# Optimization experiments

Hardware: AMD Instinct MI355X
Metric: run time of the kernel (lower is better)

The kernel has to match this reference:

```python
import jax, jax.numpy as jnp
import numpy as np

B, N, DIM = 16, 3136, 512
HEADS, AGENT, WINDOW = 8, 49, 14


def setup_inputs() -> dict:
    key = jax.random.key(0)
    ks = jax.random.split(key, 14)
    s = 0.02
    return {
        "x": jax.random.normal(ks[0], (B, N, DIM), jnp.float32),
        "w_qkv": jax.random.normal(ks[1], (3 * DIM, DIM), jnp.float32) * 0.02,
        "w_proj": jax.random.normal(ks[2], (DIM, DIM), jnp.float32) * 0.02,
        "b_proj": jnp.zeros((DIM,), jnp.float32),
        "w_dwc": jax.random.normal(ks[3], (DIM, 1, 3, 3), jnp.float32) * 0.1,
        "b_dwc": jnp.zeros((DIM,), jnp.float32),
        "an_bias": jax.random.normal(ks[4], (HEADS, AGENT, 7, 7), jnp.float32) * s,
        "na_bias": jax.random.normal(ks[5], (HEADS, AGENT, 7, 7), jnp.float32) * s,
        "ah_bias": jax.random.normal(ks[6], (1, HEADS, AGENT, WINDOW, 1), jnp.float32) * s,
        "aw_bias": jax.random.normal(ks[7], (1, HEADS, AGENT, 1, WINDOW), jnp.float32) * s,
        "ha_bias": jax.random.normal(ks[8], (1, HEADS, WINDOW, 1, AGENT), jnp.float32) * s,
        "wa_bias": jax.random.normal(ks[9], (1, HEADS, 1, WINDOW, AGENT), jnp.float32) * s,
        "ca_bias": jax.random.normal(ks[10], (1, HEADS, 1, AGENT), jnp.float32) * s,
    }


def reference(x, w_qkv, w_proj, b_proj, w_dwc, b_dwc, an_bias, na_bias,
              ah_bias, aw_bias, ha_bias, wa_bias, ca_bias):
    b, n, c = x.shape
    h = w = int(np.sqrt(n))            # 56x56, static
    nh, hd = HEADS, c // HEADS
    scale = hd ** -0.5
    ww = WINDOW * WINDOW               # 196

    qkv = x @ w_qkv.T                  # (b, n, 3c)
    q, k, v = jnp.split(qkv, 3, axis=-1)

    # agent tokens: adaptive avg-pool q to (7, 7)  (exact block mean, 56/7=8)
    pool = int(AGENT ** 0.5)
    q_img = q.reshape(b, h, w, c).transpose(0, 3, 1, 2)  # (b, c, h, w)
    pooled = q_img.reshape(b, c, pool, h // pool, pool, w // pool).mean(axis=(3, 5))
    agent = pooled.reshape(b, c, AGENT).transpose(0, 2, 1)  # (b, 49, c)

    qh = q.reshape(b, n, nh, hd).transpose(0, 2, 1, 3)      # (b, H, n, d)
    kh = k.reshape(b, n, nh, hd).transpose(0, 2, 1, 3)
    vh = v.reshape(b, n, nh, hd).transpose(0, 2, 1, 3)
    ah = agent.reshape(b, AGENT, nh, hd).transpose(0, 2, 1, 3)  # (b, H, 49, d)

    # ---- stage 1: agent -> kv attention ----
    pb1 = jax.image.resize(an_bias, (nh, AGENT, WINDOW, WINDOW), 'bilinear')
    pb1 = pb1.reshape(1, nh, AGENT, ww)
    pb2 = (ah_bias + aw_bias).reshape(1, nh, AGENT, ww)
    pb = jnp.broadcast_to(pb1 + pb2, (b, nh, AGENT, ww))
    scores1 = jnp.einsum('bhad,bhnd->bhan', ah * scale, kh)     # (b, H, 49, n)
    pb_up = jax.image.resize(pb, scores1.shape, 'bilinear')     # 196 -> n along last dim
    attn1 = jax.nn.softmax(scores1 + pb_up, axis=-1)
    agent_v = jnp.einsum('bhan,bhnd->bhad', attn1, vh)          # (b, H, 49, d)

    # ---- stage 2: query -> agent attention ----
    ab1 = jax.image.resize(na_bias, (nh, AGENT, WINDOW, WINDOW), 'bilinear')
    ab1 = ab1.reshape(1, nh, AGENT, ww).transpose(0, 1, 3, 2)   # (1, H, 196, 49)
    ab2 = (ha_bias + wa_bias).reshape(1, nh, ww, AGENT)
    ab = jnp.broadcast_to(ab1 + ab2, (b, nh, ww, AGENT))
    ab = jnp.concatenate([jnp.broadcast_to(ca_bias, (b, nh, 1, AGENT)), ab], axis=-2)
    scores2 = jnp.einsum('bhnd,bhad->bhna', qh * scale, ah)     # (b, H, n, 49)
    ab_up = jax.image.resize(ab, scores2.shape, 'bilinear')     # 197 -> n along dim -2
    attn2 = jax.nn.softmax(scores2 + ab_up, axis=-1)
    out = jnp.einsum('bhna,bhad->bhnd', attn2, agent_v)
    out = out.transpose(0, 2, 1, 3).reshape(b, n, c)

    # ---- depthwise-conv residual on v ----
    v_img = vh.transpose(0, 2, 1, 3).reshape(b, h, w, c).transpose(0, 3, 1, 2)
    dwc = jax.lax.conv_general_dilated(
        v_img, w_dwc, (1, 1), 'SAME',
        dimension_numbers=('NCHW', 'OIHW', 'NCHW'), feature_group_count=c)
    dwc = dwc + b_dwc[None, :, None, None]
    out = out + dwc.transpose(0, 2, 3, 1).reshape(b, n, c)

    return out @ w_proj.T + b_proj
```

## Files before the change

### kernel.cpp

```cpp
#include <hip/hip_runtime.h>

typedef unsigned short u16;
typedef unsigned int   u32;
typedef unsigned long long u64;
typedef float  f32x4  __attribute__((ext_vector_type(4)));
typedef __bf16 bf16x8 __attribute__((ext_vector_type(8)));

#define DEV static __device__ __forceinline__

DEV float bf2f(u16 u){ union{float f;u32 i;}v; v.i=((u32)u)<<16; return v.f; }
DEV float bflo(u32 u){ union{float f;u32 i;}v; v.i=u<<16; return v.f; }
DEV float bfhi(u32 u){ union{float f;u32 i;}v; v.i=u&0xffff0000u; return v.f; }
DEV u16   f2bf(float f){ union{float f;u32 i;}v; v.f=f; return (u16)((v.i + 0x7fffu + ((v.i>>16)&1u))>>16); }

DEV void async16(const void* g, void* l){
  __builtin_amdgcn_global_load_lds((const __attribute__((address_space(1))) void*)g,
                                   (__attribute__((address_space(3))) void*)l, 16, 0, 0);
}

__global__ __launch_bounds__(256) void cast_bf16(const float* __restrict__ in,
                                                 u16* __restrict__ out, int n4)
{
  int i = blockIdx.x*256 + threadIdx.x;
  if (i >= n4) return;
  float4 v = ((const float4*)in)[i];
  ushort4 o;
  o.x = f2bf(v.x); o.y = f2bf(v.y); o.z = f2bf(v.z); o.w = f2bf(v.w);
  ((ushort4*)out)[i] = o;
}

__global__ __launch_bounds__(256) void gemm_bt(
    const u16* __restrict__ A, const u16* __restrict__ W, int K, int mode,
    u16* __restrict__ oq, u16* __restrict__ okk, u16* __restrict__ ov,
    float* __restrict__ of, const float* __restrict__ bias)
{
  __shared__ __align__(16) u16 As[4096];
  __shared__ __align__(16) u16 Bs[4096];
  const int tid  = threadIdx.x;
  const int wave = tid >> 6, lane = tid & 63;
  const int wm = wave >> 1, wn = wave & 1;
  const int r16 = lane & 15, q4 = lane >> 4;
  const size_t Abase = (size_t)blockIdx.x * 128 * K;
  const size_t Bbase = (size_t)blockIdx.y * 128 * K;

  f32x4 acc[4][4];
  #pragma unroll
  for (int i=0;i<4;i++)
    #pragma unroll
    for (int j=0;j<4;j++) acc[i][j] = (f32x4){0.f,0.f,0.f,0.f};

  for (int k0 = 0; k0 < K; k0 += 32) {
    #pragma unroll
    for (int i=0;i<2;i++){
      int c   = wave*128 + i*64 + lane;
      int row = c >> 2, kc = (c & 3) * 8;
      async16(A + Abase + (size_t)row*K + k0 + kc, (char*)As + (wave*128 + i*64)*16);
      async16(W + Bbase + (size_t)row*K + k0 + kc, (char*)Bs + (wave*128 + i*64)*16);
    }
    __syncthreads();
    bf16x8 af[4], bfr[4];
    #pragma unroll
    for (int i=0;i<4;i++) af[i]  = *(const bf16x8*)&As[(wm*64 + i*16 + r16)*32 + q4*8];
    #pragma unroll
    for (int j=0;j<4;j++) bfr[j] = *(const bf16x8*)&Bs[(wn*64 + j*16 + r16)*32 + q4*8];
    #pragma unroll
    for (int i=0;i<4;i++)
      #pragma unroll
      for (int j=0;j<4;j++)
        acc[i][j] = __builtin_amdgcn_mfma_f32_16x16x32_bf16(af[i], bfr[j], acc[i][j], 0,0,0);
    __syncthreads();
  }

  const int m0 = blockIdx.x*128 + wm*64;
  const int n0 = blockIdx.y*128 + wn*64;
  #pragma unroll
  for (int i=0;i<4;i++)
    #pragma unroll
    for (int j=0;j<4;j++)
      #pragma unroll
      for (int r=0;r<4;r++){
        int m = m0 + i*16 + q4*4 + r;
        int n = n0 + j*16 + r16;
        float val = acc[i][j][r];
        if (mode == 0){
          int sel = n >> 9, col = n & 511;
          u16* dst = sel==0 ? oq : (sel==1 ? okk : ov);
          dst[(size_t)m*512 + col] = f2bf(val);
        } else {
          of[(size_t)m*512 + n] = val + bias[n];
        }
      }
}

__global__ __launch_bounds__(256) void pool_q(const u16* __restrict__ qb, u16* __restrict__ agentb)
{
  int idx = blockIdx.x*256 + threadIdx.x;
  int c = idx & 511;
  int ba = idx >> 9;
  int a = ba & 63, b = ba >> 6;
  if (a >= 49) { agentb[idx] = 0; return; }
  int ay = a / 7, ax = a % 7;
  const u16* base = qb + (size_t)b*3136*512 + c;
  float acc = 0.f;
  #pragma unroll
  for (int iy=0; iy<8; iy++){
    int rowoff = ((ay*8 + iy)*56 + ax*8) * 512;
    #pragma unroll
    for (int ix=0; ix<8; ix++) acc += bf2f(base[(size_t)rowoff + ix*512]);
  }
  agentb[idx] = f2bf(acc * 0.015625f);
}

DEV void lin1(float c, int S, int& i0, int& i1, float& w){
  if (c <= 0.f){ i0=0; i1=0; w=0.f; }
  else if (c >= (float)(S-1)){ i0=S-1; i1=S-1; w=0.f; }
  else { i0=(int)c; i1=i0+1; w=c-(float)i0; }
}
DEV float bilin7(const float* s, int Y, int X){
  int y0,y1,x0,x1; float wy,wx;
  lin1(0.5f*Y - 0.25f, 7, y0,y1,wy);
  lin1(0.5f*X - 0.25f, 7, x0,x1,wx);
  float v0 = s[y0*7+x0] + wx*(s[y0*7+x1]-s[y0*7+x0]);
  float v1 = s[y1*7+x0] + wx*(s[y1*7+x1]-s[y1*7+x0]);
  return v0 + wy*(v1 - v0);
}
__global__ __launch_bounds__(256) void bias_pre(
    const float* __restrict__ an_bias, const float* __restrict__ na_bias,
    const float* __restrict__ ah_bias, const float* __restrict__ aw_bias,
    const float* __restrict__ ha_bias, const float* __restrict__ wa_bias,
    const float* __restrict__ ca_bias, float* __restrict__ PB, float* __restrict__ AB)
{
  int idx = blockIdx.x*256 + threadIdx.x;
  if (idx < 8*49*196){
    int j = idx % 196; int ha = idx / 196; int a = ha % 49, h = ha / 49;
    int wy = j / 14, wx = j % 14;
    PB[idx] = bilin7(an_bias + (h*49+a)*49, wy, wx)
            + ah_bias[(h*49+a)*14 + wy] + aw_bias[(h*49+a)*14 + wx];
  }
  int idx2 = idx - 8*49*196;
  if (idx2 >= 0 && idx2 < 8*197*49){
    int a = idx2 % 49; int hr = idx2 / 49; int r = hr % 197, h = hr / 197;
    float v;
    if (r == 0) v = ca_bias[h*49 + a];
    else {
      int j = r - 1; int wy = j / 14, wx = j % 14;
      v = bilin7(na_bias + (h*49+a)*49, wy, wx)
        + ha_bias[(h*14+wy)*49 + a] + wa_bias[(h*14+wx)*49 + a];
    }
    AB[idx2] = v;
  }
}

__global__ __launch_bounds__(256) void pbit_expand(const float* __restrict__ PB, float* __restrict__ PBIT)
{
  int idx = blockIdx.x*256 + threadIdx.x;
  if (idx >= 1605632) return;
  int a = idx & 63; int t = idx >> 6; int n = t % 3136; int h = t / 3136;
  float val = -1e30f;
  if (a < 49) {
    const float* row = PB + (h*49 + a)*196;
    float c1 = (n + 0.5f)*0.0625f - 0.5f;
    if (c1 <= 0.f) val = row[0];
    else if (c1 >= 195.f) val = row[195];
    else { int j0 = (int)c1; float w = c1 - (float)j0; val = row[j0] + w*(row[j0+1]-row[j0]); }
  }
  PBIT[idx] = val;
}

__global__ __launch_bounds__(256) void abi_expand(const float* __restrict__ AB, float* __restrict__ ABI)
{
  int idx = blockIdx.x*256 + threadIdx.x;
  if (idx >= 1605632) return;
  int a = idx & 63; int t = idx >> 6; int n = t % 3136; int h = t / 3136;
  float val = -1e30f;
  if (a < 49) {
    float c2 = (n + 0.5f)*(197.0f/3136.0f) - 0.5f;
    int r0; float w;
    if (c2 <= 0.f) { r0 = 0; w = 0.f; }
    else if (c2 >= 196.f) { r0 = 196; w = 0.f; }
    else { r0 = (int)c2; w = c2 - (float)r0; }
    int r1 = (r0 < 196) ? r0 + 1 : 196;
    float v0 = AB[(h*197 + r0)*49 + a];
    float v1 = AB[(h*197 + r1)*49 + a];
    val = v0 + w*(v1 - v0);
  }
  ABI[idx] = val;
}

__global__ __launch_bounds__(256) void stage1_mfma(
    const u16* __restrict__ kb, const u16* __restrict__ vb,
    const u16* __restrict__ agentb, const float* __restrict__ PBIT,
    float* __restrict__ pav, float* __restrict__ psum)
{
  int bh = blockIdx.x, chunk = blockIdx.y;
  int b = bh >> 3, h = bh & 7;
  int tid = threadIdx.x, lane = tid & 63, w = tid >> 6;
  int r16 = lane & 15, q4 = lane >> 4;
  __shared__ __align__(16) u16 kld[64*64];
  __shared__ __align__(16) u16 vt[64*68];
  __shared__ __align__(16) u16 scb[64*72];

  int agent = w*16 + r16;
  bf16x8 bah[2];
  {
    const u16* ap = agentb + ((size_t)(b*64 + agent))*512 + h*64 + q4*8;
    bah[0] = *(const bf16x8*)ap;
    bah[1] = *(const bf16x8*)(ap + 32);
  }
  f32x4 Oacc[4];
  #pragma unroll
  for (int nt = 0; nt < 4; nt++) Oacc[nt] = (f32x4){0.f,0.f,0.f,0.f};
  float ssum = 0.f;
  int n0 = chunk * 448;
  const u16* kbase = kb + ((size_t)b*3136)*512 + h*64;
  const u16* vbase = vb + ((size_t)b*3136)*512 + h*64;

  for (int it = 0; it < 7; it++) {
    int nt0 = n0 + it*64;
    __syncthreads();
    #pragma unroll
    for (int i = 0; i < 2; i++) {
      int L = w*128 + i*64 + lane;
      int row = L >> 3, colc = (L & 7) ^ (row & 7);
      async16(kbase + (size_t)(nt0 + row)*512 + colc*8, (char*)kld + (w*128 + i*64)*16);
    }
    uint4 va[2]; int vtok[2], vdc[2];
    #pragma unroll
    for (int i = 0; i < 2; i++) {
      int c = tid + i*256;
      vtok[i] = c >> 3; vdc[i] = (c & 7)*8;
      va[i] = *(const uint4*)(vbase + (size_t)(nt0 + vtok[i])*512 + vdc[i]);
    }
    #pragma unroll
    for (int i = 0; i < 2; i++) {
      u32 uu[4] = {va[i].x, va[i].y, va[i].z, va[i].w};
      #pragma unroll
      for (int e = 0; e < 4; e++) {
        vt[(vdc[i] + 2*e + 0)*68 + vtok[i]] = (u16)(uu[e] & 0xffffu);
        vt[(vdc[i] + 2*e + 1)*68 + vtok[i]] = (u16)(uu[e] >> 16);
      }
    }
    __syncthreads();
    f32x4 S[4];
    #pragma unroll
    for (int mt = 0; mt < 4; mt++) S[mt] = (f32x4){0.f,0.f,0.f,0.f};
    #pragma unroll
    for (int ks = 0; ks < 2; ks++)
      #pragma unroll
      for (int mt = 0; mt < 4; mt++) {
        int row = mt*16 + r16;
        int colc = (ks*4 + q4) ^ (row & 7);
        bf16x8 afr = *(const bf16x8*)&kld[row*64 + colc*8];
        S[mt] = __builtin_amdgcn_mfma_f32_16x16x32_bf16(afr, bah[ks], S[mt], 0,0,0);
      }
    #pragma unroll
    for (int mt = 0; mt < 4; mt++) {
      u64 pk = 0;
      #pragma unroll
      for (int r = 0; r < 4; r++) {
        int tokl = mt*16 + q4*4 + r;
        float bias = PBIT[((size_t)h*3136 + nt0 + tokl)*64 + agent];
        float e = __expf(0.125f*S[mt][r] + bias);
        ssum += e;
        pk |= ((u64)f2bf(e)) << (16*r);
      }
      *(u64*)&scb[agent*72 + mt*16 + q4*4] = pk;
    }
    #pragma unroll
    for (int ks = 0; ks < 2; ks++) {
      bf16x8 ap = *(const bf16x8*)&scb[agent*72 + ks*32 + q4*8];
      #pragma unroll
      for (int nt = 0; nt < 4; nt++) {
        union { bf16x8 v; uint2 u[2]; } bb;
        int dim = nt*16 + r16;
        bb.u[0] = *(const uint2*)&vt[dim*68 + ks*32 + q4*8];
        bb.u[1] = *(const uint2*)&vt[dim*68 + ks*32 + q4*8 + 4];
        Oacc[nt] = __builtin_amdgcn_mfma_f32_16x16x32_bf16(ap, bb.v, Oacc[nt], 0,0,0);
      }
    }
  }
  ssum += __shfl_xor(ssum, 16);
  ssum += __shfl_xor(ssum, 32);
  size_t pb = (size_t)chunk*128 + bh;
  #pragma unroll
  for (int nt = 0; nt < 4; nt++)
    #pragma unroll
    for (int r = 0; r < 4; r++)
      pav[(pb*64 + (w*16 + q4*4 + r))*64 + nt*16 + r16] = Oacc[nt][r];
  if (lane < 16) psum[pb*64 + w*16 + lane] = ssum;
}

__global__ __launch_bounds__(256) void reduce_agv(
    const float* __restrict__ pav, const float* __restrict__ psum, u16* __restrict__ avTg)
{
  int idx = blockIdx.x*256 + threadIdx.x;
  int d = idx & 63, a = (idx >> 6) & 63, bh = idx >> 12;
  float val = 0.f;
  if (a < 49) {
    float acc = 0.f, s = 0.f;
    #pragma unroll
    for (int c = 0; c < 7; c++) {
      acc += pav[(((size_t)c*128 + bh)*64 + a)*64 + d];
      s   += psum[((size_t)c*128 + bh)*64 + a];
    }
    val = acc / s;
  }
  avTg[((size_t)bh*64 + d)*72 + a] = f2bf(val);
}

__global__ __launch_bounds__(256) void stage2_mfma(
    const u16* __restrict__ qb, const u16* __restrict__ agentb,
    const u16* __restrict__ avTg, const float* __restrict__ ABI,
    u16* __restrict__ aout)
{
  int bh = blockIdx.x, chunk = blockIdx.y;
  int b = bh >> 3, h = bh & 7;
  int tid = threadIdx.x, lane = tid & 63, w = tid >> 6;
  int r16 = lane & 15, q4 = lane >> 4;
  __shared__ __align__(16) u16 avs[64*72];
  __shared__ __align__(16) u16 scb2[4*16*72];

  const u16* avsrc = avTg + (size_t)bh*4608;
  #pragma unroll
  for (int rr = 0; rr < 3; rr++) {
    int c = rr*256 + w*64 + lane;
    if (c < 576) async16(avsrc + c*8, (char*)avs + ((size_t)rr*256 + w*64)*16);
  }
  bf16x8 bah[4][2];
  #pragma unroll
  for (int nt = 0; nt < 4; nt++) {
    const u16* ap = agentb + ((size_t)(b*64 + nt*16 + r16))*512 + h*64 + q4*8;
    bah[nt][0] = *(const bf16x8*)ap;
    bah[nt][1] = *(const bf16x8*)(ap + 32);
  }
  __syncthreads();

  u16* scw = scb2 + w*16*72;
  for (int t = 0; t < 7; t++) {
    int tok0 = (chunk*28 + w*7 + t)*16;
    bf16x8 aq[2];
    {
      const u16* qp = qb + ((size_t)b*3136 + tok0 + r16)*512 + h*64 + q4*8;
      aq[0] = *(const bf16x8*)qp;
      aq[1] = *(const bf16x8*)(qp + 32);
    }
    f32x4 S[4];
    #pragma unroll
    for (int nt = 0; nt < 4; nt++) S[nt] = (f32x4){0.f,0.f,0.f,0.f};
    #pragma unroll
    for (int ks = 0; ks < 2; ks++)
      #pragma unroll
      for (int nt = 0; nt < 4; nt++)
        S[nt] = __builtin_amdgcn_mfma_f32_16x16x32_bf16(aq[ks], bah[nt][ks], S[nt], 0,0,0);
    float rs[4] = {0.f,0.f,0.f,0.f};
    #pragma unroll
    for (int nt = 0; nt < 4; nt++)
      #pragma unroll
      for (int r = 0; r < 4; r++) {
        int tokl = q4*4 + r;
        float bias = ABI[((size_t)h*3136 + tok0 + tokl)*64 + nt*16 + r16];
        float e = __expf(0.125f*S[nt][r] + bias);
        rs[r] += e;
        scw[tokl*72 + nt*16 + r16] = f2bf(e);
      }
    #pragma unroll
    for (int m = 1; m <= 8; m <<= 1)
      #pragma unroll
      for (int r = 0; r < 4; r++) rs[r] += __shfl_xor(rs[r], m);
    f32x4 O[4];
    #pragma unroll
    for (int nt = 0; nt < 4; nt++) O[nt] = (f32x4){0.f,0.f,0.f,0.f};
    #pragma unroll
    for (int ks = 0; ks < 2; ks++) {
      bf16x8 ap2 = *(const bf16x8*)&scw[r16*72 + ks*32 + q4*8];
      #pragma unroll
      for (int nt = 0; nt < 4; nt++) {
        bf16x8 bv = *(const bf16x8*)&avs[(nt*16 + r16)*72 + ks*32 + q4*8];
        O[nt] = __builtin_amdgcn_mfma_f32_16x16x32_bf16(ap2, bv, O[nt], 0,0,0);
      }
    }
    float inv[4];
    #pragma unroll
    for (int r = 0; r < 4; r++) inv[r] = 1.0f / rs[r];
    #pragma unroll
    for (int nt = 0; nt < 4; nt++)
      #pragma unroll
      for (int r = 0; r < 4; r++)
        aout[((size_t)b*3136 + tok0 + q4*4 + r)*512 + h*64 + nt*16 + r16] = f2bf(O[nt][r]*inv[r]);
  }
}

__global__ __launch_bounds__(256) void dwc_add2(
    const u16* __restrict__ vb, const float* __restrict__ w_dwc,
    const float* __restrict__ b_dwc, u16* __restrict__ io)
{
  int wave = (blockIdx.x << 2) + (threadIdx.x >> 6);
  int lane = threadIdx.x & 63;
  int c0 = lane * 8;

  float wt[9][8];
  {
    float tmp[72];
    const float4* wp = (const float4*)(w_dwc + c0*9);
    #pragma unroll
    for (int i = 0; i < 18; i++) {
      float4 v4 = wp[i];
      tmp[4*i] = v4.x; tmp[4*i+1] = v4.y; tmp[4*i+2] = v4.z; tmp[4*i+3] = v4.w;
    }
    #pragma unroll
    for (int j = 0; j < 8; j++)
      #pragma unroll
      for (int tp = 0; tp < 9; tp++) wt[tp][j] = tmp[j*9 + tp];
  }
  float bias[8];
  {
    const float4* bp = (const float4*)(b_dwc + c0);
    float4 a4 = bp[0], b4 = bp[1];
    bias[0]=a4.x; bias[1]=a4.y; bias[2]=a4.z; bias[3]=a4.w;
    bias[4]=b4.x; bias[5]=b4.y; bias[6]=b4.z; bias[7]=b4.w;
  }

  int t0 = wave * 16;
  int b = t0 / 3136;
  int n0 = t0 - b*3136;
  const u16* vbase = vb + ((size_t)b*3136)*512 + c0;

  for (int ti = 0; ti < 16; ti++) {
    int n = n0 + ti;
    int y = n / 56, x = n - y*56;
    size_t toff = ((size_t)b*3136 + n)*512 + c0;
    float acc[8];
    {
      uint4 uo = *(const uint4*)(io + toff);
      u32 uu[4] = {uo.x, uo.y, uo.z, uo.w};
      #pragma unroll
      for (int e = 0; e < 4; e++) {
        acc[2*e+0] = bflo(uu[e]) + bias[2*e+0];
        acc[2*e+1] = bfhi(uu[e]) + bias[2*e+1];
      }
    }
    #pragma unroll
    for (int dy = 0; dy < 3; dy++) {
      int yy = y + dy - 1;
      if (yy < 0 || yy > 55) continue;
      #pragma unroll
      for (int dx = 0; dx < 3; dx++) {
        int xx = x + dx - 1;
        if (xx < 0 || xx > 55) continue;
        uint4 uv = *(const uint4*)(vbase + ((size_t)(yy*56 + xx) << 9));
        u32 uu[4] = {uv.x, uv.y, uv.z, uv.w};
        const float* wr = wt[dy*3 + dx];
        #pragma unroll
        for (int e = 0; e < 4; e++) {
          acc[2*e+0] += bflo(uu[e]) * wr[2*e+0];
          acc[2*e+1] += bfhi(uu[e]) * wr[2*e+1];
        }
      }
    }
    uint4 pk;
    pk.x = (u32)f2bf(acc[0]) | ((u32)f2bf(acc[1]) << 16);
    pk.y = (u32)f2bf(acc[2]) | ((u32)f2bf(acc[3]) << 16);
    pk.z = (u32)f2bf(acc[4]) | ((u32)f2bf(acc[5]) << 16);
    pk.w = (u32)f2bf(acc[6]) | ((u32)f2bf(acc[7]) << 16);
    *(uint4*)(io + toff) = pk;
  }
}

extern "C" void kernel_launch(void* const* d_in, const int* in_sizes, int n_in,
                              void* d_out, int out_size, void* d_ws, size_t ws_size,
                              hipStream_t stream)
{
  const float* x       = (const float*)d_in[0];
  const float* w_qkv   = (const float*)d_in[1];
  const float* w_proj  = (const float*)d_in[2];
  const float* b_proj  = (const float*)d_in[3];
  const float* w_dwc   = (const float*)d_in[4];
  const float* b_dwc   = (const float*)d_in[5];
  const float* an_bias = (const float*)d_in[6];
  const float* na_bias = (const float*)d_in[7];
  const float* ah_bias = (const float*)d_in[8];
  const float* aw_bias = (const float*)d_in[9];
  const float* ha_bias = (const float*)d_in[10];
  const float* wa_bias = (const float*)d_in[11];
  const float* ca_bias = (const float*)d_in[12];

  if (ws_size < 210000000u) return;

  char* p = (char*)d_ws;
  u16* regA   = (u16*)p;  p += 51380224;
  u16* qb     = (u16*)p;  p += 51380224;
  u16* kb     = (u16*)p;  p += 51380224;
  u16* vb     = (u16*)p;  p += 51380224;
  u16* wqkvb  = (u16*)p;  p += 1572864;
  u16* wprojb = (u16*)p;  p += 524288;
  u16* agentb = (u16*)p;  p += 1048576;
  float* PB   = (float*)p; p += 307456;
  float* AB   = (float*)p; p += 309248;

  float* PBIT = (float*)((char*)regA);
  float* ABI  = (float*)((char*)regA + 6422528);
  float* pav  = (float*)((char*)regA + 12845056);
  float* psum = (float*)((char*)regA + 27525120);
  u16*   avTg = (u16*)  ((char*)regA + 27754496);
  u16*   aout = kb;

  cast_bf16<<<25088, 256, 0, stream>>>(x, regA, 6422528);
  cast_bf16<<<768,   256, 0, stream>>>(w_qkv, wqkvb, 196608);
  cast_bf16<<<256,   256, 0, stream>>>(w_proj, wprojb, 65536);

  gemm_bt<<<dim3(392,12), 256, 0, stream>>>(regA, wqkvb, 512, 0, qb, kb, vb, nullptr, nullptr);
  pool_q<<<2048, 256, 0, stream>>>(qb, agentb);
  bias_pre<<<602, 256, 0, stream>>>(an_bias, na_bias, ah_bias, aw_bias, ha_bias, wa_bias, ca_bias, PB, AB);
  pbit_expand<<<6272, 256, 0, stream>>>(PB, PBIT);
  abi_expand<<<6272, 256, 0, stream>>>(AB, ABI);
  stage1_mfma<<<dim3(128,7), 256, 0, stream>>>(kb, vb, agentb, PBIT, pav, psum);
  reduce_agv<<<2048, 256, 0, stream>>>(pav, psum, avTg);
  stage2_mfma<<<dim3(128,7), 256, 0, stream>>>(qb, agentb, avTg, ABI, aout);
  dwc_add2<<<784, 256, 0, stream>>>(vb, w_dwc, b_dwc, aout);
  gemm_bt<<<dim3(392,4), 256, 0, stream>>>(aout, wprojb, 512, 1, nullptr, nullptr, nullptr,
                                           (float*)d_out, b_proj);
}
```

Measured before the change: 554.2 us.

## Deepen GEMM K-tile with XOR-swizzled LDS, vectorize epilogue stores, merge bias expands

The shared GEMM now stages a 64-wide K slice per iteration, halving the number of barriers. It uses an XOR swizzle on the LDS column chunks to avoid bank conflicts on the fragment reads. MFMA operands are swapped so each lane holds four consecutive output columns, letting the epilogue write packed bf16x4 or float4 stores instead of scalar ones. The two bias-expansion kernels are merged into one launch. LDS per block doubles to 32 KB, which may reduce occupancy.

```diff
diff --git a/kernel.cpp b/kernel.cpp
--- a/kernel.cpp
+++ b/kernel.cpp
@@ -34,12 +34,13 @@
     u16* __restrict__ oq, u16* __restrict__ okk, u16* __restrict__ ov,
     float* __restrict__ of, const float* __restrict__ bias)
 {
-  __shared__ __align__(16) u16 As[4096];
-  __shared__ __align__(16) u16 Bs[4096];
+  __shared__ __align__(16) u16 As[8192];
+  __shared__ __align__(16) u16 Bs[8192];
   const int tid  = threadIdx.x;
   const int wave = tid >> 6, lane = tid & 63;
   const int wm = wave >> 1, wn = wave & 1;
   const int r16 = lane & 15, q4 = lane >> 4;
+  const int xr = r16 & 7;
   const size_t Abase = (size_t)blockIdx.x * 128 * K;
   const size_t Bbase = (size_t)blockIdx.y * 128 * K;
 
@@ -49,47 +50,64 @@
     #pragma unroll
     for (int j=0;j<4;j++) acc[i][j] = (f32x4){0.f,0.f,0.f,0.f};
 
-  for (int k0 = 0; k0 < K; k0 += 32) {
-    #pragma unroll
-    for (int i=0;i<2;i++){
-      int c   = wave*128 + i*64 + lane;
-      int row = c >> 2, kc = (c & 3) * 8;
-      async16(A + Abase + (size_t)row*K + k0 + kc, (char*)As + (wave*128 + i*64)*16);
-      async16(W + Bbase + (size_t)row*K + k0 + kc, (char*)Bs + (wave*128 + i*64)*16);
+  for (int k0 = 0; k0 < K; k0 += 64) {
+    #pragma unroll
+    for (int i=0;i<4;i++){
+      int s   = i*256 + tid;
+      int row = s >> 3;
+      int c   = (s & 7) ^ (row & 7);
+      async16(A + Abase + (size_t)row*K + k0 + c*8, (char*)As + (size_t)s*16);
+      async16(W + Bbase + (size_t)row*K + k0 + c*8, (char*)Bs + (size_t)s*16);
     }
     __syncthreads();
-    bf16x8 af[4], bfr[4];
-    #pragma unroll
-    for (int i=0;i<4;i++) af[i]  = *(const bf16x8*)&As[(wm*64 + i*16 + r16)*32 + q4*8];
-    #pragma unroll
-    for (int j=0;j<4;j++) bfr[j] = *(const bf16x8*)&Bs[(wn*64 + j*16 + r16)*32 + q4*8];
-    #pragma unroll
-    for (int i=0;i<4;i++)
-      #pragma unroll
-      for (int j=0;j<4;j++)
-        acc[i][j] = __builtin_amdgcn_mfma_f32_16x16x32_bf16(af[i], bfr[j], acc[i][j], 0,0,0);
+    #pragma unroll
+    for (int ks=0; ks<2; ks++){
+      const int xo = ((ks*4 + q4) ^ xr) * 8;
+      bf16x8 af[4], bfr[4];
+      #pragma unroll
+      for (int i=0;i<4;i++) af[i]  = *(const bf16x8*)&As[(wm*64 + i*16 + r16)*64 + xo];
+      #pragma unroll
+      for (int j=0;j<4;j++) bfr[j] = *(const bf16x8*)&Bs[(wn*64 + j*16 + r16)*64 + xo];
+      #pragma unroll
+      for (int i=0;i<4;i++)
+        #pragma unroll
+        for (int j=0;j<4;j++)
+          acc[i][j] = __builtin_amdgcn_mfma_f32_16x16x32_bf16(bfr[j], af[i], acc[i][j], 0,0,0);
+    }
     __syncthreads();
   }
 
   const int m0 = blockIdx.x*128 + wm*64;
   const int n0 = blockIdx.y*128 + wn*64;
-  #pragma unroll
-  for (int i=0;i<4;i++)
-    #pragma unroll
-    for (int j=0;j<4;j++)
-      #pragma unroll
-      for (int r=0;r<4;r++){
-        int m = m0 + i*16 + q4*4 + r;
-        int n = n0 + j*16 + r16;
-        float val = acc[i][j][r];
-        if (mode == 0){
-          int sel = n >> 9, col = n & 511;
-          u16* dst = sel==0 ? oq : (sel==1 ? okk : ov);
-          dst[(size_t)m*512 + col] = f2bf(val);
-        } else {
-          of[(size_t)m*512 + n] = val + bias[n];
-        }
-      }
+  if (mode == 0){
+    int sel = blockIdx.y >> 2;
+    u16* dst = sel==0 ? oq : (sel==1 ? okk : ov);
+    #pragma unroll
+    for (int i=0;i<4;i++){
+      int token = m0 + i*16 + r16;
+      #pragma unroll
+      for (int j=0;j<4;j++){
+        int col = (n0 + j*16 + q4*4) & 511;
+        uint2 pk;
+        pk.x = (u32)f2bf(acc[i][j][0]) | ((u32)f2bf(acc[i][j][1]) << 16);
+        pk.y = (u32)f2bf(acc[i][j][2]) | ((u32)f2bf(acc[i][j][3]) << 16);
+        *(uint2*)&dst[(size_t)token*512 + col] = pk;
+      }
+    }
+  } else {
+    #pragma unroll
+    for (int j=0;j<4;j++){
+      int nbase = n0 + j*16 + q4*4;
+      float4 b4 = *(const float4*)&bias[nbase];
+      #pragma unroll
+      for (int i=0;i<4;i++){
+        int token = m0 + i*16 + r16;
+        float4 o4 = { acc[i][j][0]+b4.x, acc[i][j][1]+b4.y,
+                      acc[i][j][2]+b4.z, acc[i][j][3]+b4.w };
+        *(float4*)&of[(size_t)token*512 + nbase] = o4;
+      }
+    }
+  }
 }
 
 __global__ __launch_bounds__(256) void pool_q(const u16* __restrict__ qb, u16* __restrict__ agentb)
@@ -151,40 +169,40 @@
   }
 }
 
-__global__ __launch_bounds__(256) void pbit_expand(const float* __restrict__ PB, float* __restrict__ PBIT)
+__global__ __launch_bounds__(256) void bias_expand2(
+    const float* __restrict__ PB, const float* __restrict__ AB,
+    float* __restrict__ PBIT, float* __restrict__ ABI)
 {
   int idx = blockIdx.x*256 + threadIdx.x;
-  if (idx >= 1605632) return;
-  int a = idx & 63; int t = idx >> 6; int n = t % 3136; int h = t / 3136;
-  float val = -1e30f;
-  if (a < 49) {
-    const float* row = PB + (h*49 + a)*196;
-    float c1 = (n + 0.5f)*0.0625f - 0.5f;
-    if (c1 <= 0.f) val = row[0];
-    else if (c1 >= 195.f) val = row[195];
-    else { int j0 = (int)c1; float w = c1 - (float)j0; val = row[j0] + w*(row[j0+1]-row[j0]); }
-  }
-  PBIT[idx] = val;
-}
-
-__global__ __launch_bounds__(256) void abi_expand(const float* __restrict__ AB, float* __restrict__ ABI)
-{
-  int idx = blockIdx.x*256 + threadIdx.x;
-  if (idx >= 1605632) return;
-  int a = idx & 63; int t = idx >> 6; int n = t % 3136; int h = t / 3136;
-  float val = -1e30f;
-  if (a < 49) {
-    float c2 = (n + 0.5f)*(197.0f/3136.0f) - 0.5f;
-    int r0; float w;
-    if (c2 <= 0.f) { r0 = 0; w = 0.f; }
-    else if (c2 >= 196.f) { r0 = 196; w = 0.f; }
-    else { r0 = (int)c2; w = c2 - (float)r0; }
-    int r1 = (r0 < 196) ? r0 + 1 : 196;
-    float v0 = AB[(h*197 + r0)*49 + a];
-    float v1 = AB[(h*197 + r1)*49 + a];
-    val = v0 + w*(v1 - v0);
-  }
-  ABI[idx] = val;
+  if (idx < 1605632) {
+    int a = idx & 63; int t = idx >> 6; int n = t % 3136; int h = t / 3136;
+    float val = -1e30f;
+    if (a < 49) {
+      const float* row = PB + (h*49 + a)*196;
+      float c1 = (n + 0.5f)*0.0625f - 0.5f;
+      if (c1 <= 0.f) val = row[0];
+      else if (c1 >= 195.f) val = row[195];
+      else { int j0 = (int)c1; float w = c1 - (float)j0; val = row[j0] + w*(row[j0+1]-row[j0]); }
+    }
+    PBIT[idx] = val;
+  } else {
+    int idx2 = idx - 1605632;
+    if (idx2 >= 1605632) return;
+    int a = idx2 & 63; int t = idx2 >> 6; int n = t % 3136; int h = t / 3136;
+    float val = -1e30f;
+    if (a < 49) {
+      float c2 = (n + 0.5f)*(197.0f/3136.0f) - 0.5f;
+      int r0; float w;
+      if (c2 <= 0.f) { r0 = 0; w = 0.f; }
+      else if (c2 >= 196.f) { r0 = 196; w = 0.f; }
+      else { r0 = (int)c2; w = c2 - (float)r0; }
+      int r1 = (r0 < 196) ? r0 + 1 : 196;
+      float v0 = AB[(h*197 + r0)*49 + a];
+      float v1 = AB[(h*197 + r1)*49 + a];
+      val = v0 + w*(v1 - v0);
+    }
+    ABI[idx2] = val;
+  }
 }
 
 __global__ __launch_bounds__(256) void stage1_mfma(
@@ -511,8 +529,7 @@
   gemm_bt<<<dim3(392,12), 256, 0, stream>>>(regA, wqkvb, 512, 0, qb, kb, vb, nullptr, nullptr);
   pool_q<<<2048, 256, 0, stream>>>(qb, agentb);
   bias_pre<<<602, 256, 0, stream>>>(an_bias, na_bias, ah_bias, aw_bias, ha_bias, wa_bias, ca_bias, PB, AB);
-  pbit_expand<<<6272, 256, 0, stream>>>(PB, PBIT);
-  abi_expand<<<6272, 256, 0, stream>>>(AB, ABI);
+  bias_expand2<<<12544, 256, 0, stream>>>(PB, AB, PBIT, ABI);
   stage1_mfma<<<dim3(128,7), 256, 0, stream>>>(kb, vb, agentb, PBIT, pav, psum);
   reduce_agv<<<2048, 256, 0, stream>>>(pav, psum, avTg);
   stage2_mfma<<<dim3(128,7), 256, 0, stream>>>(qb, agentb, avTg, ABI, aout);
```

New measurement: 547.3 us. About the same (-1.2%).
